# Kernel optimization log

Hardware: AMD Instinct MI355X
Metric: run time of the kernel (lower is better)

## Reference

```python
import jax, jax.numpy as jnp
import numpy as np

N = 50000        # nodes
E = 1_000_000    # edges
F_IN = 128       # input features
H1, D1 = 8, 16   # layer-1 heads / per-head dim
D2 = 2           # layer-2 out dim (heads=1, concat=False)
NEG_SLOPE = 0.2  # PyG GATConv default leaky-relu slope


def setup_inputs() -> dict:
    key = jax.random.key(0)
    ks = jax.random.split(key, 10)
    x = jax.random.normal(ks[0], (N, F_IN), dtype=jnp.float32)
    edge_index = jax.random.randint(ks[1], (2, E), 0, N, dtype=jnp.int32)
    # layer 1 params: W1 maps F_IN -> H1*D1; attention vectors per head
    W1 = jax.random.normal(ks[2], (F_IN, H1 * D1), jnp.float32) * 0.1
    a_src1 = jax.random.normal(ks[3], (H1, D1), jnp.float32) * 0.1
    a_dst1 = jax.random.normal(ks[4], (H1, D1), jnp.float32) * 0.1
    b1 = jnp.zeros((H1 * D1,), jnp.float32)
    # layer 2 params: 128 -> 2, single head
    W2 = jax.random.normal(ks[5], (H1 * D1, 1 * D2), jnp.float32) * 0.1
    a_src2 = jax.random.normal(ks[6], (1, D2), jnp.float32) * 0.1
    a_dst2 = jax.random.normal(ks[7], (1, D2), jnp.float32) * 0.1
    b2 = jnp.zeros((D2,), jnp.float32)
    return {"x": x, "edge_index": edge_index,
            "W1": W1, "a_src1": a_src1, "a_dst1": a_dst1, "b1": b1,
            "W2": W2, "a_src2": a_src2, "a_dst2": a_dst2, "b2": b2}


def gat_layer(x, src, dst, W, a_s, a_d, b, concat):
    # PyG GATConv: h = xW (per head); e_ij = leaky_relu(a_s.h_j + a_d.h_i);
    # alpha = softmax over incoming edges of node i; out_i = sum alpha_ij h_j
    n = x.shape[0]
    heads, d = a_s.shape
    h = (x @ W).reshape(n, heads, d)                      # [N,H,D]
    es = jnp.einsum('nhd,hd->nh', h, a_s)                 # [N,H]
    ed = jnp.einsum('nhd,hd->nh', h, a_d)
    e = jax.nn.leaky_relu(es[src] + ed[dst], NEG_SLOPE)   # [E,H]
    m = jax.ops.segment_max(e, dst, num_segments=n)       # stable softmax max
    m = jnp.where(jnp.isfinite(m), m, 0.0)
    w = jnp.exp(e - m[dst])
    denom = jax.ops.segment_sum(w, dst, num_segments=n)
    alpha = w / (denom[dst] + 1e-16)                      # [E,H]
    out = jax.ops.segment_sum(alpha[:, :, None] * h[src], dst, num_segments=n)
    out = out.reshape(n, heads * d) if concat else out.mean(axis=1)
    return out + b


def reference(x, edge_index, W1, a_src1, a_dst1, b1, W2, a_src2, a_dst2, b2):
    n = x.shape[0]
    loops = jnp.arange(n, dtype=edge_index.dtype)         # add_self_loops (PyG default)
    src = jnp.concatenate([edge_index[0], loops])
    dst = jnp.concatenate([edge_index[1], loops])
    x1 = jax.nn.elu(gat_layer(x, src, dst, W1, a_src1, a_dst1, b1, concat=True))
    x2 = jax.nn.elu(gat_layer(x1, src, dst, W2, a_src2, a_dst2, b2, concat=False))
    return x2.mean(axis=0)                                # [2]
```

## Files before the change

### kernel.cpp

```cpp
#include <hip/hip_runtime.h>
#include <hip/hip_fp8.h>
#include <math.h>

#define NEG_SLOPE 0.2f
#define FD 128
#define H1 8
#define BSH 7
#define BWD 128
#define CAPE 3072
#define CAPC 3200
#define SCAP 3200
#define CHK 2048
#define XPAD 136
#define LOG2E 1.44269504088896f

#if defined(__has_builtin)
#if __has_builtin(__builtin_amdgcn_cvt_pk_f32_fp8) && __has_builtin(__builtin_amdgcn_cvt_pk_fp8_f32)
#define HW_FP8 1
#endif
#if __has_builtin(__builtin_amdgcn_exp2f)
#define HW_EXP2 1
#endif
#endif

typedef float v2f __attribute__((ext_vector_type(2)));
typedef short bf16x8 __attribute__((ext_vector_type(8)));
typedef float f32x4v __attribute__((ext_vector_type(4)));

__device__ inline float fexp2(float x) {
#ifdef HW_EXP2
    return __builtin_amdgcn_exp2f(x);
#else
    return exp2f(x);
#endif
}

__device__ inline unsigned char fp8_1(float v) {
#ifdef HW_FP8
    return (unsigned char)(__builtin_amdgcn_cvt_pk_fp8_f32(v, v, 0, false) & 0xff);
#else
    __hip_fp8_e4m3 q(v); return (unsigned char)q.__x;
#endif
}

template <bool HI>
__device__ inline v2f unpack2_fp8(unsigned int pk) {
#ifdef HW_FP8
    return __builtin_amdgcn_cvt_pk_f32_fp8((int)pk, HI);
#else
    __hip_fp8_e4m3 q0, q1;
    const int sh = HI ? 16 : 0;
    q0.__x = (__hip_fp8_storage_t)((pk >> sh) & 0xff);
    q1.__x = (__hip_fp8_storage_t)((pk >> (sh + 8)) & 0xff);
    v2f r; r.x = (float)q0; r.y = (float)q1;
    return r;
#endif
}

__device__ inline unsigned int pkbf2(float a, float b) {
    union { float f; unsigned u; } ua, ub;
    ua.f = a; ub.f = b;
    unsigned ra = (ua.u + 0x7FFF + ((ua.u >> 16) & 1)) >> 16;
    unsigned rb = (ub.u + 0x7FFF + ((ub.u >> 16) & 1)) >> 16;
    return (ra & 0xFFFFu) | (rb << 16);
}


__global__ __launch_bounds__(256) void prep_kernel(
        const float* __restrict__ W1, unsigned short* __restrict__ W1t,
        int* __restrict__ cur, int nbk) {
    int t = blockIdx.x * 256 + threadIdx.x;
    if (t < FD * FD) {
        int k = t >> 7, n = t & 127;
        union { float f; unsigned u; } uu;
        uu.f = W1[t];
        unsigned r = (uu.u + 0x7FFF + ((uu.u >> 16) & 1)) >> 16;
        W1t[n * FD + k] = (unsigned short)r;
    }
    if (t < nbk) cur[t] = t * CAPE;
}

union FusedSmem {
    struct {
        unsigned short xs[64 * XPAD];
        unsigned short wt[128 * XPAD];
    } g;
    int bucket[1024];
};

__global__ __launch_bounds__(256) void fused_gemm_bucketize_kernel(
        const float* __restrict__ x, const unsigned short* __restrict__ W1t,
        const float* __restrict__ a_s, const float* __restrict__ a_d,
        unsigned char* __restrict__ h1, float* __restrict__ es1, float* __restrict__ ed1,
        int N, const int* __restrict__ ei, int E, int nbk,
        int* __restrict__ bkt_cursor, int* __restrict__ bkt_edges, int nchk) {
    __shared__ FusedSmem sm;
    const int tid = threadIdx.x;

    if ((int)blockIdx.x < nchk) {
        int* lcnt = sm.bucket;
        int* lbase = sm.bucket + nbk;
        for (int i = tid; i < nbk; i += 256) lcnt[i] = 0;
        __syncthreads();
        const int base = blockIdx.x * CHK;
        const int end = min(base + CHK, E);
        int info[CHK / 256];
        #pragma unroll
        for (int t = 0; t < CHK / 256; t++) {
            int i = base + tid + t * 256;
            info[t] = -1;
            if (i < end) {
                int b = ei[E + i] >> BSH;
                int r = atomicAdd(&lcnt[b], 1);
                info[t] = (r << 9) | b;
            }
        }
        __syncthreads();
        for (int i = tid; i < nbk; i += 256) {
            int c = lcnt[i];
            lbase[i] = c ? atomicAdd(&bkt_cursor[i], c) : 0;
        }
        __syncthreads();
        #pragma unroll
        for (int t = 0; t < CHK / 256; t++) {
            int i = base + tid + t * 256;
            if (info[t] >= 0) {
                int b = info[t] & 511;
                int r = info[t] >> 9;
                int pos = lbase[b] + r;
                if (pos < (b + 1) * CAPE) {
                    unsigned int src = (unsigned int)ei[i];
                    unsigned int dl = (unsigned int)(ei[E + i] & (BWD - 1));
                    bkt_edges[pos] = (int)(src | (dl << 25));
                }
            }
        }
        return;
    }

    const int tile = blockIdx.x - nchk;
    const int row0 = tile * 64;
    unsigned short* xs = sm.g.xs;
    unsigned short* wt = sm.g.wt;

    #pragma unroll
    for (int it = 0; it < 8; ++it) {
        int idx = it * 256 + tid;
        int r   = idx >> 5;
        int c4  = idx & 31;
        int gr  = min(row0 + r, N - 1);
        float4 v = ((const float4*)(x + (size_t)gr * FD))[c4];
        unsigned int p0 = pkbf2(v.x, v.y);
        unsigned int p1 = pkbf2(v.z, v.w);
        *(unsigned int*)(xs + r * XPAD + c4 * 4) = p0;
        *(unsigned int*)(xs + r * XPAD + c4 * 4 + 2) = p1;
    }
    #pragma unroll
    for (int it = 0; it < 8; ++it) {
        int idx = it * 256 + tid;
        int n = idx >> 4, k8 = (idx & 15) * 8;
        int4 v = *(const int4*)(W1t + n * FD + k8);
        *(int4*)(wt + n * XPAD + k8) = v;
    }
    __syncthreads();

    const int wave = tid >> 6, lane = tid & 63;
    const int quad = lane >> 4, l16 = lane & 15;
    const int n0w = wave * 32;

    f32x4v acc[4][2];
    #pragma unroll
    for (int mt = 0; mt < 4; mt++)
        #pragma unroll
        for (int nt = 0; nt < 2; nt++)
            #pragma unroll
            for (int c = 0; c < 4; c++) acc[mt][nt][c] = 0.f;

    #pragma unroll
    for (int kt = 0; kt < 4; kt++) {
        const int kb = kt * 32 + quad * 8;
        bf16x8 a0 = *(const bf16x8*)(xs + (0 * 16 + l16) * XPAD + kb);
        bf16x8 a1 = *(const bf16x8*)(xs + (1 * 16 + l16) * XPAD + kb);
        bf16x8 a2 = *(const bf16x8*)(xs + (2 * 16 + l16) * XPAD + kb);
        bf16x8 a3 = *(const bf16x8*)(xs + (3 * 16 + l16) * XPAD + kb);
        bf16x8 b0 = *(const bf16x8*)(wt + (n0w + 0 * 16 + l16) * XPAD + kb);
        bf16x8 b1 = *(const bf16x8*)(wt + (n0w + 1 * 16 + l16) * XPAD + kb);
        acc[0][0] = __builtin_amdgcn_mfma_f32_16x16x32_bf16(a0, b0, acc[0][0], 0, 0, 0);
        acc[1][0] = __builtin_amdgcn_mfma_f32_16x16x32_bf16(a1, b0, acc[1][0], 0, 0, 0);
        acc[2][0] = __builtin_amdgcn_mfma_f32_16x16x32_bf16(a2, b0, acc[2][0], 0, 0, 0);
        acc[3][0] = __builtin_amdgcn_mfma_f32_16x16x32_bf16(a3, b0, acc[3][0], 0, 0, 0);
        acc[0][1] = __builtin_amdgcn_mfma_f32_16x16x32_bf16(a0, b1, acc[0][1], 0, 0, 0);
        acc[1][1] = __builtin_amdgcn_mfma_f32_16x16x32_bf16(a1, b1, acc[1][1], 0, 0, 0);
        acc[2][1] = __builtin_amdgcn_mfma_f32_16x16x32_bf16(a2, b1, acc[2][1], 0, 0, 0);
        acc[3][1] = __builtin_amdgcn_mfma_f32_16x16x32_bf16(a3, b1, acc[3][1], 0, 0, 0);
    }

    #pragma unroll
    for (int nt = 0; nt < 2; nt++) {
        const int col = n0w + nt * 16 + l16;
        const int head = wave * 2 + nt;
        const float asv = a_s[col];
        const float adv = a_d[col];
        #pragma unroll
        for (int mt = 0; mt < 4; mt++) {
            #pragma unroll
            for (int reg = 0; reg < 4; reg++) {
                int row = row0 + mt * 16 + quad * 4 + reg;
                float v = acc[mt][nt][reg];
                float ps = v * asv, pd = v * adv;
                ps += __shfl_xor(ps, 1, 16); pd += __shfl_xor(pd, 1, 16);
                ps += __shfl_xor(ps, 2, 16); pd += __shfl_xor(pd, 2, 16);
                ps += __shfl_xor(ps, 4, 16); pd += __shfl_xor(pd, 4, 16);
                ps += __shfl_xor(ps, 8, 16); pd += __shfl_xor(pd, 8, 16);
                if (row < N) {
                    h1[(size_t)row * FD + col] = fp8_1(v);
                    if (l16 == 0) {
                        es1[row * H1 + head] = ps * LOG2E;
                        ed1[row * H1 + head] = pd * LOG2E;
                    }
                }
            }
        }
    }
}

__global__ __launch_bounds__(256) void sort2_kernel(
        const int* __restrict__ bkt_cursor, const int* __restrict__ bkt_edges,
        int* __restrict__ csr_src, int* __restrict__ rowstart,
        int* __restrict__ rowend, int N) {
    __shared__ int lcnt[BWD];
    __shared__ int lcur[BWD];
    __shared__ int stage[SCAP];
    __shared__ int sorted[SCAP];
    const int b = blockIdx.x;
    const int n0 = b << BSH;
    const int nb = min(BWD, N - n0);
    const int s = b * CAPE;
    const int cnt = min(bkt_cursor[b] - s, CAPE);
    const int region = b * CAPC;
    const int tid = threadIdx.x;

    if (tid < BWD) lcnt[tid] = (tid < nb) ? 1 : 0;
    __syncthreads();
    for (int i = tid; i < cnt; i += 256) {
        int v = bkt_edges[s + i];
        stage[i] = v;
        atomicAdd(&lcnt[((unsigned int)v) >> 25], 1);
    }
    __syncthreads();
    if (tid < 64) {
        int carry = 0;
        #pragma unroll
        for (int half = 0; half < 2; half++) {
            int i = half * 64 + tid;
            int v = lcnt[i];
            int incl = v;
            #pragma unroll
            for (int off = 1; off < 64; off <<= 1) {
                int t = __shfl_up(incl, off);
                if (tid >= off) incl += t;
            }
            lcur[i] = carry + incl - v;
            carry += __shfl(incl, 63);
        }
    }
    __syncthreads();
    if (tid < nb) {
        int p = lcur[tid];
        rowstart[n0 + tid] = region + p;
        rowend[n0 + tid] = region + p + lcnt[tid];
        sorted[p] = n0 + tid;
        lcur[tid] = p + 1;
    }
    __syncthreads();
    for (int i = tid; i < cnt; i += 256) {
        int v = stage[i];
        int dl = ((unsigned int)v) >> 25;
        int src = v & 0x1FFFFFF;
        int pos = atomicAdd(&lcur[dl], 1);
        sorted[pos] = src;
    }
    __syncthreads();
    const int total = cnt + nb;
    for (int i = total + tid; i < CAPC; i += 256) sorted[i] = 0;
    __syncthreads();
    int4* dst4 = (int4*)(csr_src + region);
    const int4* src4 = (const int4*)sorted;
    for (int i = tid; i < CAPC / 4; i += 256) dst4[i] = src4[i];
}

__global__ __launch_bounds__(64) void agg1_kernel(
        const unsigned int* __restrict__ h1, const float* __restrict__ es1,
        const float* __restrict__ ed1,
        const int* __restrict__ rowstart, const int* __restrict__ rowend,
        const int* __restrict__ csr_src,
        const float* __restrict__ b1, const float* __restrict__ W2,
        const float* __restrict__ a_s2, const float* __restrict__ a_d2,
        float* __restrict__ h2, float* __restrict__ es2, float* __restrict__ ed2, int N) {
    const int j = threadIdx.x;
    const int q = j & 31;
    const int h = q >> 2;
    const int n = blockIdx.x * 2 + (j >> 5);
    const bool valid = (n < N);

    int s = 0, e = 0;
    float edh = 0.f;
    if (valid) {
        s = rowstart[n];
        e = rowend[n];
        edh = ed1[(n << 3) + h];
    }
    int nbat = (e - s + 31) >> 5;
    int nmax = max(nbat, __shfl_xor(nbat, 32));

    float acc0 = 0.f, acc1 = 0.f, acc2 = 0.f, acc3 = 0.f, wsum = 0.f;
    for (int k = 0; k < nmax; ++k) {
        int base = s + (k << 5);
        int cm = min(e - base, 32);
        int myidx = csr_src[base + q];
        myidx = min(max(myidx, 0), N - 1);
        int cl = max(cm - 1, 0);
        int cmax = max(cm, __shfl_xor(cm, 32));
        for (int t = 0; t < cmax; t += 8) {
            int i0 = min(t, cl),     i1 = min(t + 1, cl);
            int i2 = min(t + 2, cl), i3 = min(t + 3, cl);
            int i4 = min(t + 4, cl), i5 = min(t + 5, cl);
            int i6 = min(t + 6, cl), i7 = min(t + 7, cl);
            int s0 = __shfl(myidx, i0, 32);
            int s1 = __shfl(myidx, i1, 32);
            int s2 = __shfl(myidx, i2, 32);
            int s3 = __shfl(myidx, i3, 32);
            int s4 = __shfl(myidx, i4, 32);
            int s5 = __shfl(myidx, i5, 32);
            int s6 = __shfl(myidx, i6, 32);
            int s7 = __shfl(myidx, i7, 32);
            float g0 = es1[(s0 << 3) + h];
            float g1 = es1[(s1 << 3) + h];
            float g2 = es1[(s2 << 3) + h];
            float g3 = es1[(s3 << 3) + h];
            float g4 = es1[(s4 << 3) + h];
            float g5 = es1[(s5 << 3) + h];
            float g6 = es1[(s6 << 3) + h];
            float g7 = es1[(s7 << 3) + h];
            unsigned int p0 = h1[(s0 << 5) + q];
            unsigned int p1 = h1[(s1 << 5) + q];
            unsigned int p2 = h1[(s2 << 5) + q];
            unsigned int p3 = h1[(s3 << 5) + q];
            unsigned int p4 = h1[(s4 << 5) + q];
            unsigned int p5 = h1[(s5 << 5) + q];
            unsigned int p6 = h1[(s6 << 5) + q];
            unsigned int p7 = h1[(s7 << 5) + q];
            g0 += edh; g1 += edh; g2 += edh; g3 += edh;
            g4 += edh; g5 += edh; g6 += edh; g7 += edh;
            g0 = fmaxf(g0, g0 * NEG_SLOPE);
            g1 = fmaxf(g1, g1 * NEG_SLOPE);
            g2 = fmaxf(g2, g2 * NEG_SLOPE);
            g3 = fmaxf(g3, g3 * NEG_SLOPE);
            g4 = fmaxf(g4, g4 * NEG_SLOPE);
            g5 = fmaxf(g5, g5 * NEG_SLOPE);
            g6 = fmaxf(g6, g6 * NEG_SLOPE);
            g7 = fmaxf(g7, g7 * NEG_SLOPE);
            float w0 = (t     < cm) ? fexp2(g0) : 0.f;
            float w1 = (t + 1 < cm) ? fexp2(g1) : 0.f;
            float w2 = (t + 2 < cm) ? fexp2(g2) : 0.f;
            float w3 = (t + 3 < cm) ? fexp2(g3) : 0.f;
            float w4 = (t + 4 < cm) ? fexp2(g4) : 0.f;
            float w5 = (t + 5 < cm) ? fexp2(g5) : 0.f;
            float w6 = (t + 6 < cm) ? fexp2(g6) : 0.f;
            float w7 = (t + 7 < cm) ? fexp2(g7) : 0.f;
            v2f a01 = unpack2_fp8<false>(p0), a23 = unpack2_fp8<true>(p0);
            v2f b01 = unpack2_fp8<false>(p1), b23 = unpack2_fp8<true>(p1);
            v2f c01 = unpack2_fp8<false>(p2), c23 = unpack2_fp8<true>(p2);
            v2f d01 = unpack2_fp8<false>(p3), d23 = unpack2_fp8<true>(p3);
            v2f e01 = unpack2_fp8<false>(p4), e23 = unpack2_fp8<true>(p4);
            v2f f01 = unpack2_fp8<false>(p5), f23 = unpack2_fp8<true>(p5);
            v2f g01 = unpack2_fp8<false>(p6), g23 = unpack2_fp8<true>(p6);
            v2f h01 = unpack2_fp8<false>(p7), h23 = unpack2_fp8<true>(p7);
            acc0 += w0 * a01.x; acc1 += w0 * a01.y; acc2 += w0 * a23.x; acc3 += w0 * a23.y;
            acc0 += w1 * b01.x; acc1 += w1 * b01.y; acc2 += w1 * b23.x; acc3 += w1 * b23.y;
            acc0 += w2 * c01.x; acc1 += w2 * c01.y; acc2 += w2 * c23.x; acc3 += w2 * c23.y;
            acc0 += w3 * d01.x; acc1 += w3 * d01.y; acc2 += w3 * d23.x; acc3 += w3 * d23.y;
            acc0 += w4 * e01.x; acc1 += w4 * e01.y; acc2 += w4 * e23.x; acc3 += w4 * e23.y;
            acc0 += w5 * f01.x; acc1 += w5 * f01.y; acc2 += w5 * f23.x; acc3 += w5 * f23.y;
            acc0 += w6 * g01.x; acc1 += w6 * g01.y; acc2 += w6 * g23.x; acc3 += w6 * g23.y;
            acc0 += w7 * h01.x; acc1 += w7 * h01.y; acc2 += w7 * h23.x; acc3 += w7 * h23.y;
            wsum += (w0 + w1) + (w2 + w3) + (w4 + w5) + (w6 + w7);
        }
    }

    float inv = 1.f / wsum;
    float4 bv = *(const float4*)&b1[4 * q];
    float x0 = acc0 * inv + bv.x;
    float x1 = acc1 * inv + bv.y;
    float x2 = acc2 * inv + bv.z;
    float x3 = acc3 * inv + bv.w;
    x0 = (x0 > 0.f) ? x0 : expm1f(x0);
    x1 = (x1 > 0.f) ? x1 : expm1f(x1);
    x2 = (x2 > 0.f) ? x2 : expm1f(x2);
    x3 = (x3 > 0.f) ? x3 : expm1f(x3);

    float4 w2a = *(const float4*)&W2[8 * q];
    float4 w2b = *(const float4*)&W2[8 * q + 4];
    float c0 = x0 * w2a.x + x1 * w2a.z + x2 * w2b.x + x3 * w2b.z;
    float c1 = x0 * w2a.y + x1 * w2a.w + x2 * w2b.y + x3 * w2b.w;
    #pragma unroll
    for (int m = 1; m < 32; m <<= 1) {
        c0 += __shfl_xor(c0, m);
        c1 += __shfl_xor(c1, m);
    }
    if (q == 0 && valid) {
        h2[(size_t)n * 2 + 0] = c0;
        h2[(size_t)n * 2 + 1] = c1;
        es2[n] = LOG2E * (c0 * a_s2[0] + c1 * a_s2[1]);
        ed2[n] = LOG2E * (c0 * a_d2[0] + c1 * a_d2[1]);
    }
}

__global__ __launch_bounds__(256) void agg2_kernel(
        const float* __restrict__ h2, const float* __restrict__ es2, const float* __restrict__ ed2,
        const int* __restrict__ rowstart, const int* __restrict__ rowend,
        const int* __restrict__ csr_src,
        const float* __restrict__ b2, float* __restrict__ partial, int N) {
    const int g = threadIdx.x >> 5, lane = threadIdx.x & 31;
    const int n = blockIdx.x * 8 + g;
    float v0 = 0.f, v1 = 0.f;
    if (n < N) {
        const float ed = ed2[n];
        const int s = rowstart[n], e = rowend[n];
        float a0 = 0.f, a1 = 0.f, ws = 0.f;
        for (int i = s + lane; i < e; i += 32) {
            int src = csr_src[i];
            float t = es2[src] + ed;
            float w = fexp2(fmaxf(t, t * NEG_SLOPE));
            a0 += w * h2[(size_t)src * 2 + 0];
            a1 += w * h2[(size_t)src * 2 + 1];
            ws += w;
        }
        #pragma unroll
        for (int m = 1; m < 32; m <<= 1) {
            a0 += __shfl_xor(a0, m, 32);
            a1 += __shfl_xor(a1, m, 32);
            ws += __shfl_xor(ws, m, 32);
        }
        if (lane == 0) {
            v0 = a0 / ws + b2[0]; v0 = (v0 > 0.f) ? v0 : expm1f(v0);
            v1 = a1 / ws + b2[1]; v1 = (v1 > 0.f) ? v1 : expm1f(v1);
        }
    }
    __shared__ float buf[16];
    if (lane == 0) { buf[g * 2] = v0; buf[g * 2 + 1] = v1; }
    __syncthreads();
    if (threadIdx.x == 0) {
        float s0 = 0.f, s1 = 0.f;
        #pragma unroll
        for (int i = 0; i < 8; i++) { s0 += buf[2 * i]; s1 += buf[2 * i + 1]; }
        partial[(size_t)blockIdx.x * 2 + 0] = s0;
        partial[(size_t)blockIdx.x * 2 + 1] = s1;
    }
}

__global__ __launch_bounds__(256) void final_reduce_kernel(
        const float* __restrict__ partial, int nb, float invN, float* __restrict__ out) {
    const int tid = threadIdx.x, lane = tid & 63, wv = tid >> 6;
    float s0 = 0.f, s1 = 0.f;
    for (int i = tid; i < nb; i += 256) { s0 += partial[2 * i]; s1 += partial[2 * i + 1]; }
    #pragma unroll
    for (int m = 1; m < 64; m <<= 1) { s0 += __shfl_xor(s0, m); s1 += __shfl_xor(s1, m); }
    __shared__ float buf[8];
    if (lane == 0) { buf[wv * 2] = s0; buf[wv * 2 + 1] = s1; }
    __syncthreads();
    if (tid == 0) {
        out[0] = (buf[0] + buf[2] + buf[4] + buf[6]) * invN;
        out[1] = (buf[1] + buf[3] + buf[5] + buf[7]) * invN;
    }
}

extern "C" void kernel_launch(void* const* d_in, const int* in_sizes, int n_in,
                              void* d_out, int out_size, void* d_ws, size_t ws_size,
                              hipStream_t stream) {
    const float* x    = (const float*)d_in[0];
    const int*   ei   = (const int*)  d_in[1];
    const float* W1   = (const float*)d_in[2];
    const float* a_s1 = (const float*)d_in[3];
    const float* a_d1 = (const float*)d_in[4];
    const float* b1   = (const float*)d_in[5];
    const float* W2   = (const float*)d_in[6];
    const float* a_s2 = (const float*)d_in[7];
    const float* a_d2 = (const float*)d_in[8];
    const float* b2   = (const float*)d_in[9];
    float* out = (float*)d_out;

    const int N = in_sizes[0] / FD;
    const int E = in_sizes[1] / 2;
    const int nbk  = (N + BWD - 1) >> BSH;
    const int nchk = (E + CHK - 1) / CHK;
    const int ngemm = (N + 63) / 64;

    char* wp = (char*)d_ws;
    auto carve = [&](size_t bytes) {
        char* p = wp;
        wp += (bytes + 255) & ~(size_t)255;
        return p;
    };
    unsigned char* h1 = (unsigned char*)carve((size_t)N * FD);
    float* es1      = (float*)carve((size_t)N * H1 * 4);
    float* ed1      = (float*)carve((size_t)N * H1 * 4);
    int*   rowstart = (int*)  carve((size_t)N * 4);
    int*   rowend   = (int*)  carve((size_t)N * 4);
    int*   csr_src  = (int*)  carve(((size_t)nbk * CAPC + CAPC) * 4);
    int*   bkt_cursor = (int*)carve((size_t)nbk * 4);
    int*   bkt_edges  = (int*)carve((size_t)nbk * CAPE * 4);
    unsigned short* W1t = (unsigned short*)carve((size_t)FD * FD * 2);
    float* h2       = (float*)carve((size_t)N * 2 * 4);
    float* es2      = (float*)carve((size_t)N * 4);
    float* ed2      = (float*)carve((size_t)N * 4);
    const int nb2   = (N + 7) / 8;
    float* partial  = (float*)carve((size_t)nb2 * 2 * 4);

    prep_kernel<<<(FD * FD + 255) / 256, 256, 0, stream>>>(W1, W1t, bkt_cursor, nbk);

    fused_gemm_bucketize_kernel<<<nchk + ngemm, 256, 0, stream>>>(
        x, W1t, a_s1, a_d1, h1, es1, ed1, N, ei, E, nbk, bkt_cursor, bkt_edges, nchk);

    sort2_kernel<<<nbk, 256, 0, stream>>>(bkt_cursor, bkt_edges, csr_src, rowstart, rowend, N);

    agg1_kernel<<<(N + 1) / 2, 64, 0, stream>>>((const unsigned int*)h1, es1, ed1,
                                                rowstart, rowend, csr_src,
                                                b1, W2, a_s2, a_d2, h2, es2, ed2, N);

    agg2_kernel<<<(N + 7) / 8, 256, 0, stream>>>(h2, es2, ed2, rowstart, rowend, csr_src,
                                                 b2, partial, N);
    final_reduce_kernel<<<1, 256, 0, stream>>>(partial, nb2, 1.0f / (float)N, out);
}
```

Baseline: 185.5 us.

## Fold attention vectors into weights and compute scores via extra MFMA

Precomputes W1·a_src and W1·a_dst (scaled by log2e) in the prep kernel as hi/lo bf16 pairs, so the GEMM kernel gets the per-head attention scores from an extra MFMA per wave. This replaces the per-element shuffle reductions in the epilogue. It also stops staging W1t in shared memory and reads B fragments straight from global/L2, which shrinks shared memory use and may raise occupancy. The risks are extra global-load latency in the inner loop and a slightly different numeric path for the scores, which now come from x in bf16 times folded weights rather than from the fp32 GEMM output.

```diff
diff --git a/kernel.cpp b/kernel.cpp
--- a/kernel.cpp
+++ b/kernel.cpp
@@ -65,9 +65,16 @@
     return (ra & 0xFFFFu) | (rb << 16);
 }
 
+__device__ inline unsigned short bf16_1(float a) {
+    union { float f; unsigned u; } ua; ua.f = a;
+    return (unsigned short)((ua.u + 0x7FFF + ((ua.u >> 16) & 1)) >> 16);
+}
+
 
 __global__ __launch_bounds__(256) void prep_kernel(
-        const float* __restrict__ W1, unsigned short* __restrict__ W1t,
+        const float* __restrict__ W1, const float* __restrict__ a_s,
+        const float* __restrict__ a_d,
+        unsigned short* __restrict__ W1t, unsigned short* __restrict__ wsd,
         int* __restrict__ cur, int nbk) {
     int t = blockIdx.x * 256 + threadIdx.x;
     if (t < FD * FD) {
@@ -77,20 +84,34 @@
         unsigned r = (uu.u + 0x7FFF + ((uu.u >> 16) & 1)) >> 16;
         W1t[n * FD + k] = (unsigned short)r;
     }
+    if (t < 16 * FD) {
+        int j = t >> 7, k = t & 127;
+        int head = j & 7;
+        const float* av = (j < 8) ? (a_s + head * 16) : (a_d + head * 16);
+        const float* wr = W1 + k * FD + head * 16;
+        float v = 0.f;
+        #pragma unroll
+        for (int d = 0; d < 16; d++) v += wr[d] * av[d];
+        v *= LOG2E;
+        unsigned short hi = bf16_1(v);
+        union { float f; unsigned u; } hf; hf.u = ((unsigned)hi) << 16;
+        unsigned short lo = bf16_1(v - hf.f);
+        wsd[j * FD + k] = hi;
+        wsd[(16 + j) * FD + k] = lo;
+    }
     if (t < nbk) cur[t] = t * CAPE;
 }
 
 union FusedSmem {
     struct {
         unsigned short xs[64 * XPAD];
-        unsigned short wt[128 * XPAD];
     } g;
     int bucket[1024];
 };
 
 __global__ __launch_bounds__(256) void fused_gemm_bucketize_kernel(
         const float* __restrict__ x, const unsigned short* __restrict__ W1t,
-        const float* __restrict__ a_s, const float* __restrict__ a_d,
+        const unsigned short* __restrict__ wsd,
         unsigned char* __restrict__ h1, float* __restrict__ es1, float* __restrict__ ed1,
         int N, const int* __restrict__ ei, int E, int nbk,
         int* __restrict__ bkt_cursor, int* __restrict__ bkt_edges, int nchk) {
@@ -141,7 +162,6 @@
     const int tile = blockIdx.x - nchk;
     const int row0 = tile * 64;
     unsigned short* xs = sm.g.xs;
-    unsigned short* wt = sm.g.wt;
 
     #pragma unroll
     for (int it = 0; it < 8; ++it) {
@@ -155,13 +175,6 @@
         *(unsigned int*)(xs + r * XPAD + c4 * 4) = p0;
         *(unsigned int*)(xs + r * XPAD + c4 * 4 + 2) = p1;
     }
-    #pragma unroll
-    for (int it = 0; it < 8; ++it) {
-        int idx = it * 256 + tid;
-        int n = idx >> 4, k8 = (idx & 15) * 8;
-        int4 v = *(const int4*)(W1t + n * FD + k8);
-        *(int4*)(wt + n * XPAD + k8) = v;
-    }
     __syncthreads();
 
     const int wave = tid >> 6, lane = tid & 63;
@@ -169,12 +182,15 @@
     const int n0w = wave * 32;
 
     f32x4v acc[4][2];
+    f32x4v acce;
     #pragma unroll
     for (int mt = 0; mt < 4; mt++)
         #pragma unroll
         for (int nt = 0; nt < 2; nt++)
             #pragma unroll
             for (int c = 0; c < 4; c++) acc[mt][nt][c] = 0.f;
+    #pragma unroll
+    for (int c = 0; c < 4; c++) acce[c] = 0.f;
 
     #pragma unroll
     for (int kt = 0; kt < 4; kt++) {
@@ -183,8 +199,10 @@
         bf16x8 a1 = *(const bf16x8*)(xs + (1 * 16 + l16) * XPAD + kb);
         bf16x8 a2 = *(const bf16x8*)(xs + (2 * 16 + l16) * XPAD + kb);
         bf16x8 a3 = *(const bf16x8*)(xs + (3 * 16 + l16) * XPAD + kb);
-        bf16x8 b0 = *(const bf16x8*)(wt + (n0w + 0 * 16 + l16) * XPAD + kb);
-        bf16x8 b1 = *(const bf16x8*)(wt + (n0w + 1 * 16 + l16) * XPAD + kb);
+        bf16x8 b0 = *(const bf16x8*)(W1t + (n0w + 0 * 16 + l16) * FD + kb);
+        bf16x8 b1 = *(const bf16x8*)(W1t + (n0w + 1 * 16 + l16) * FD + kb);
+        bf16x8 bh = *(const bf16x8*)(wsd + (0 * 16 + l16) * FD + kb);
+        bf16x8 bl = *(const bf16x8*)(wsd + (1 * 16 + l16) * FD + kb);
         acc[0][0] = __builtin_amdgcn_mfma_f32_16x16x32_bf16(a0, b0, acc[0][0], 0, 0, 0);
         acc[1][0] = __builtin_amdgcn_mfma_f32_16x16x32_bf16(a1, b0, acc[1][0], 0, 0, 0);
         acc[2][0] = __builtin_amdgcn_mfma_f32_16x16x32_bf16(a2, b0, acc[2][0], 0, 0, 0);
@@ -193,32 +211,40 @@
         acc[1][1] = __builtin_amdgcn_mfma_f32_16x16x32_bf16(a1, b1, acc[1][1], 0, 0, 0);
         acc[2][1] = __builtin_amdgcn_mfma_f32_16x16x32_bf16(a2, b1, acc[2][1], 0, 0, 0);
         acc[3][1] = __builtin_amdgcn_mfma_f32_16x16x32_bf16(a3, b1, acc[3][1], 0, 0, 0);
+        if (wave == 0) {
+            acce = __builtin_amdgcn_mfma_f32_16x16x32_bf16(a0, bh, acce, 0, 0, 0);
+            acce = __builtin_amdgcn_mfma_f32_16x16x32_bf16(a0, bl, acce, 0, 0, 0);
+        } else if (wave == 1) {
+            acce = __builtin_amdgcn_mfma_f32_16x16x32_bf16(a1, bh, acce, 0, 0, 0);
+            acce = __builtin_amdgcn_mfma_f32_16x16x32_bf16(a1, bl, acce, 0, 0, 0);
+        } else if (wave == 2) {
+            acce = __builtin_amdgcn_mfma_f32_16x16x32_bf16(a2, bh, acce, 0, 0, 0);
+            acce = __builtin_amdgcn_mfma_f32_16x16x32_bf16(a2, bl, acce, 0, 0, 0);
+        } else {
+            acce = __builtin_amdgcn_mfma_f32_16x16x32_bf16(a3, bh, acce, 0, 0, 0);
+            acce = __builtin_amdgcn_mfma_f32_16x16x32_bf16(a3, bl, acce, 0, 0, 0);
+        }
+    }
+
+    #pragma unroll
+    for (int reg = 0; reg < 4; reg++) {
+        int row = row0 + wave * 16 + quad * 4 + reg;
+        if (row < N) {
+            float v = acce[reg];
+            if (l16 < 8) es1[row * H1 + l16] = v;
+            else         ed1[row * H1 + (l16 - 8)] = v;
+        }
     }
 
     #pragma unroll
     for (int nt = 0; nt < 2; nt++) {
         const int col = n0w + nt * 16 + l16;
-        const int head = wave * 2 + nt;
-        const float asv = a_s[col];
-        const float adv = a_d[col];
         #pragma unroll
         for (int mt = 0; mt < 4; mt++) {
             #pragma unroll
             for (int reg = 0; reg < 4; reg++) {
                 int row = row0 + mt * 16 + quad * 4 + reg;
-                float v = acc[mt][nt][reg];
-                float ps = v * asv, pd = v * adv;
-                ps += __shfl_xor(ps, 1, 16); pd += __shfl_xor(pd, 1, 16);
-                ps += __shfl_xor(ps, 2, 16); pd += __shfl_xor(pd, 2, 16);
-                ps += __shfl_xor(ps, 4, 16); pd += __shfl_xor(pd, 4, 16);
-                ps += __shfl_xor(ps, 8, 16); pd += __shfl_xor(pd, 8, 16);
-                if (row < N) {
-                    h1[(size_t)row * FD + col] = fp8_1(v);
-                    if (l16 == 0) {
-                        es1[row * H1 + head] = ps * LOG2E;
-                        ed1[row * H1 + head] = pd * LOG2E;
-                    }
-                }
+                if (row < N) h1[(size_t)row * FD + col] = fp8_1(acc[mt][nt][reg]);
             }
         }
     }
@@ -511,16 +537,18 @@
     int*   bkt_cursor = (int*)carve((size_t)nbk * 4);
     int*   bkt_edges  = (int*)carve((size_t)nbk * CAPE * 4);
     unsigned short* W1t = (unsigned short*)carve((size_t)FD * FD * 2);
+    unsigned short* wsd = (unsigned short*)carve((size_t)32 * FD * 2);
     float* h2       = (float*)carve((size_t)N * 2 * 4);
     float* es2      = (float*)carve((size_t)N * 4);
     float* ed2      = (float*)carve((size_t)N * 4);
     const int nb2   = (N + 7) / 8;
     float* partial  = (float*)carve((size_t)nb2 * 2 * 4);
 
-    prep_kernel<<<(FD * FD + 255) / 256, 256, 0, stream>>>(W1, W1t, bkt_cursor, nbk);
+    prep_kernel<<<(FD * FD + 255) / 256, 256, 0, stream>>>(W1, a_s1, a_d1, W1t, wsd,
+                                                           bkt_cursor, nbk);
 
     fused_gemm_bucketize_kernel<<<nchk + ngemm, 256, 0, stream>>>(
-        x, W1t, a_s1, a_d1, h1, es1, ed1, N, ei, E, nbk, bkt_cursor, bkt_edges, nchk);
+        x, W1t, wsd, h1, es1, ed1, N, ei, E, nbk, bkt_cursor, bkt_edges, nchk);
 
     sort2_kernel<<<nbk, 256, 0, stream>>>(bkt_cursor, bkt_edges, csr_src, rowstart, rowend, N);
 
```

After: 182.8 us. Within noise of the previous version (-1.5%).
